# Kernel tuning notes

Measured on AMD Instinct MI355X. Metric: run time of the kernel, lower is better.

The kernel has to match this reference:

```python
import jax, jax.numpy as jnp
import numpy as np

N, DIM, H, E = 50000, 64, 8, 800000
NEG_SLOPE = 0.2


def setup_inputs() -> dict:
    key = jax.random.key(0)
    ks = jax.random.split(key, 6)
    x = jax.random.normal(ks[0], (N, DIM), dtype=jnp.float32)
    edge_index = jax.random.randint(ks[1], (2, E), 0, N, dtype=jnp.int32)
    # glorot-ish scaled params
    W = jax.random.normal(ks[2], (DIM, H * DIM), dtype=jnp.float32) * (1.0 / np.sqrt(DIM))
    att_src = jax.random.normal(ks[3], (H, DIM), dtype=jnp.float32) * (1.0 / np.sqrt(DIM))
    att_dst = jax.random.normal(ks[4], (H, DIM), dtype=jnp.float32) * (1.0 / np.sqrt(DIM))
    bias = jnp.zeros((DIM,), dtype=jnp.float32)
    return {"x": x, "edge_index": edge_index, "W": W, "att_src": att_src, "att_dst": att_dst, "bias": bias}


def reference(x, edge_index, W, att_src, att_dst, bias):
    n = x.shape[0]
    # PyG GATConv default: add self-loops
    loops = jnp.arange(n, dtype=edge_index.dtype)
    src = jnp.concatenate([edge_index[0], loops])  # [E+N]
    dst = jnp.concatenate([edge_index[1], loops])  # [E+N]
    # project: [N, H, C]
    h = (x @ W).reshape(n, H, DIM)
    # per-node attention contributions: [N, H]
    a_src = jnp.einsum("nhc,hc->nh", h, att_src)
    a_dst = jnp.einsum("nhc,hc->nh", h, att_dst)
    # per-edge logits with LeakyReLU: [E+N, H]
    logits = jax.nn.leaky_relu(a_src[src] + a_dst[dst], negative_slope=NEG_SLOPE)
    # segment softmax over incoming edges of each destination node
    seg_max = jax.ops.segment_max(logits, dst, num_segments=n)  # [N, H]
    seg_max = jnp.where(jnp.isfinite(seg_max), seg_max, 0.0)
    e = jnp.exp(logits - seg_max[dst])
    denom = jax.ops.segment_sum(e, dst, num_segments=n)  # [N, H]
    alpha = e / denom[dst]  # every node has a self-loop -> denom > 0
    # weighted messages and scatter-add: [E+N, H, C] -> [N, H, C]
    msg = h[src] * alpha[:, :, None]
    out = jax.ops.segment_sum(msg, dst, num_segments=n)
    # concat=False -> mean over heads, then bias
    return out.mean(axis=1) + bias
```

## Files before the change

### kernel.cpp

```cpp
#include <hip/hip_runtime.h>
#include <hip/hip_bf16.h>

#define NHEAD 8
#define KDIM 64
#define NCOL 512
#define NEG_SLOPE 0.2f
#define BUCKET 64
#define EPT 8

typedef short bf16x8 __attribute__((ext_vector_type(8)));
typedef float f32x4 __attribute__((ext_vector_type(4)));

__device__ inline float leaky(float x) { return fmaxf(x, NEG_SLOPE * x); }
__device__ inline float bf2f(unsigned short u) { return __uint_as_float(((unsigned)u) << 16); }
__device__ inline unsigned short f2bf(float f) {
    unsigned b = __float_as_uint(f);
    b += 0x7FFFu + ((b >> 16) & 1u);
    return (unsigned short)(b >> 16);
}

__global__ void k_wprep(const float* __restrict__ W, const float* __restrict__ att_src,
                        const float* __restrict__ att_dst,
                        float* __restrict__ WsT, float* __restrict__ WdT,
                        unsigned short* __restrict__ Bhi, unsigned short* __restrict__ Blo) {
    int tid = blockIdx.x * 256 + threadIdx.x;
    if (tid < NHEAD * KDIM) {
        int h = tid >> 6, k = tid & 63;
        float ps = 0.f, pd = 0.f;
        const float4* wp = (const float4*)(W + (size_t)k * NCOL + h * KDIM);
        const float4* sp = (const float4*)(att_src + h * KDIM);
        const float4* dp = (const float4*)(att_dst + h * KDIM);
        #pragma unroll
        for (int q = 0; q < KDIM / 4; ++q) {
            float4 wv = wp[q], sv = sp[q], dv = dp[q];
            ps += wv.x * sv.x + wv.y * sv.y + wv.z * sv.z + wv.w * sv.w;
            pd += wv.x * dv.x + wv.y * dv.y + wv.z * dv.z + wv.w * dv.w;
        }
        WsT[h * KDIM + k] = ps;
        WdT[h * KDIM + k] = pd;
    }
    if (tid < 4 * 16 * 64 * 8) {
        int j  = tid & 7;
        int l  = (tid >> 3) & 63;
        int kk = (tid >> 9) & 15;
        int ct = tid >> 13;
        int c  = ct * 16 + (l & 15);
        int hk = kk * 32 + ((l >> 4) << 3) + j;
        int h = hk >> 6, kx = hk & 63;
        float w = W[(size_t)kx * NCOL + h * KDIM + c];
        unsigned short hi = f2bf(w);
        Bhi[tid] = hi;
        Blo[tid] = f2bf(w - bf2f(hi));
    }
}

__global__ void k_xafill(const float* __restrict__ x,
                         const int* __restrict__ src, const int* __restrict__ dst,
                         const float* __restrict__ WsT, const float* __restrict__ WdT,
                         float* __restrict__ asrc, float* __restrict__ adst,
                         unsigned short* __restrict__ xb,
                         int* __restrict__ cur, unsigned short* __restrict__ bucket,
                         int n, int E, int nbx) {
    const int b = blockIdx.x;
    const int t = threadIdx.x;
    if (b < nbx) {
        int i = b * 256 + t;
        if (i >= n * NHEAD) return;
        int node = i >> 3, h = i & 7;
        const float4* xp = (const float4*)(x + (size_t)node * KDIM);
        const float4* sp = (const float4*)(WsT + h * KDIM);
        const float4* dp = (const float4*)(WdT + h * KDIM);
        float ps = 0.f, pd = 0.f;
        float4 kept0 = {0, 0, 0, 0}, kept1 = {0, 0, 0, 0};
        #pragma unroll
        for (int q = 0; q < KDIM / 4; ++q) {
            float4 xv = xp[q], sv = sp[q], dv = dp[q];
            if (q == 2 * h)     kept0 = xv;
            if (q == 2 * h + 1) kept1 = xv;
            ps += xv.x * sv.x + xv.y * sv.y + xv.z * sv.z + xv.w * sv.w;
            pd += xv.x * dv.x + xv.y * dv.y + xv.z * dv.z + xv.w * dv.w;
        }
        asrc[i] = ps;
        adst[i] = pd;
        ushort4 o0, o1;
        o0.x = f2bf(kept0.x); o0.y = f2bf(kept0.y); o0.z = f2bf(kept0.z); o0.w = f2bf(kept0.w);
        o1.x = f2bf(kept1.x); o1.y = f2bf(kept1.y); o1.z = f2bf(kept1.z); o1.w = f2bf(kept1.w);
        ushort4* op = (ushort4*)(xb + (size_t)node * KDIM + h * 8);
        op[0] = o0; op[1] = o1;
    } else {
        long long base = ((long long)(b - nbx) * 256 + t) * EPT;
        if (base + EPT <= E) {
            int4 d0 = *(const int4*)(dst + base);
            int4 d1 = *(const int4*)(dst + base + 4);
            int4 s0 = *(const int4*)(src + base);
            int4 s1 = *(const int4*)(src + base + 4);
            int dd[EPT] = {d0.x, d0.y, d0.z, d0.w, d1.x, d1.y, d1.z, d1.w};
            int ss[EPT] = {s0.x, s0.y, s0.z, s0.w, s1.x, s1.y, s1.z, s1.w};
            int pp[EPT];
            #pragma unroll
            for (int q = 0; q < EPT; ++q) pp[q] = atomicAdd(cur + dd[q], 1);
            #pragma unroll
            for (int q = 0; q < EPT; ++q)
                if (pp[q] < BUCKET)
                    bucket[(size_t)dd[q] * BUCKET + pp[q]] = (unsigned short)ss[q];
        } else {
            for (long long i = base; i < E; ++i) {
                int d = dst[i];
                int p = atomicAdd(cur + d, 1);
                if (p < BUCKET) bucket[(size_t)d * BUCKET + p] = (unsigned short)src[i];
            }
        }
    }
}

__global__ __launch_bounds__(256, 8) void k_aggproj(const unsigned short* __restrict__ bucket,
                                                    const int* __restrict__ cur,
                                                    const float* __restrict__ asrc,
                                                    const float* __restrict__ adst,
                                                    const unsigned short* __restrict__ xb,
                                                    const unsigned short* __restrict__ Bhi,
                                                    const unsigned short* __restrict__ Blo,
                                                    const float* __restrict__ bias,
                                                    float* __restrict__ out, int n) {
    __shared__ __align__(16) unsigned short Yh_l[16][520];

    const int t = threadIdx.x;
    const int w = t >> 6;
    const int lane = t & 63;
    const int base = blockIdx.x * 16;
    const int hg = lane >> 3;
    const int dly = (lane & 7) << 3;

    for (int q = 0; q < 4; ++q) {
        const int row = w * 4 + q;
        int d = base + row;
        if (d >= n) d = n - 1;

        const float myAd = adst[(size_t)d * NHEAD + hg];
        float den = 0.f;
        float y[8];
        #pragma unroll
        for (int i = 0; i < 8; ++i) y[i] = 0.f;

#define PROCU(AV, RW)                                                          \
    {                                                                          \
        float e_ = __expf(leaky((AV) + myAd));                                 \
        den += e_;                                                             \
        uint4 u_ = (RW);                                                       \
        y[0] += e_ * __uint_as_float(u_.x << 16);                              \
        y[1] += e_ * __uint_as_float(u_.x & 0xFFFF0000u);                      \
        y[2] += e_ * __uint_as_float(u_.y << 16);                              \
        y[3] += e_ * __uint_as_float(u_.y & 0xFFFF0000u);                      \
        y[4] += e_ * __uint_as_float(u_.z << 16);                              \
        y[5] += e_ * __uint_as_float(u_.z & 0xFFFF0000u);                      \
        y[6] += e_ * __uint_as_float(u_.w << 16);                              \
        y[7] += e_ * __uint_as_float(u_.w & 0xFFFF0000u);                      \
    }

        int cnt = cur[d];
        cnt = cnt < BUCKET ? cnt : BUCKET;
        int sv = (lane < cnt) ? (int)bucket[(size_t)d * BUCKET + lane] : 0;

        {
            float a = asrc[(size_t)d * NHEAD + hg];
            uint4 r = *(const uint4*)(xb + ((size_t)d << 6) + dly);
            PROCU(a, r)
        }

        int j = 0;
        for (; j + 4 <= cnt; j += 4) {
            int s0 = __shfl(sv, j);
            int s1 = __shfl(sv, j + 1);
            int s2 = __shfl(sv, j + 2);
            int s3 = __shfl(sv, j + 3);
            float a0 = asrc[(size_t)s0 * NHEAD + hg];
            float a1 = asrc[(size_t)s1 * NHEAD + hg];
            float a2 = asrc[(size_t)s2 * NHEAD + hg];
            float a3 = asrc[(size_t)s3 * NHEAD + hg];
            uint4 r0 = *(const uint4*)(xb + ((size_t)s0 << 6) + dly);
            uint4 r1 = *(const uint4*)(xb + ((size_t)s1 << 6) + dly);
            uint4 r2 = *(const uint4*)(xb + ((size_t)s2 << 6) + dly);
            uint4 r3 = *(const uint4*)(xb + ((size_t)s3 << 6) + dly);
            PROCU(a0, r0)
            PROCU(a1, r1)
            PROCU(a2, r2)
            PROCU(a3, r3)
        }
        for (; j < cnt; ++j) {
            int s = __shfl(sv, j);
            float a = asrc[(size_t)s * NHEAD + hg];
            uint4 r = *(const uint4*)(xb + ((size_t)s << 6) + dly);
            PROCU(a, r)
        }
#undef PROCU

        float inv = 1.0f / den;
        ushort4 h0, h1;
        h0.x = f2bf(y[0] * inv); h0.y = f2bf(y[1] * inv);
        h0.z = f2bf(y[2] * inv); h0.w = f2bf(y[3] * inv);
        h1.x = f2bf(y[4] * inv); h1.y = f2bf(y[5] * inv);
        h1.z = f2bf(y[6] * inv); h1.w = f2bf(y[7] * inv);
        unsigned short* yh = &Yh_l[row][hg * KDIM + dly];
        ((ushort4*)yh)[0] = h0; ((ushort4*)yh)[1] = h1;
    }

    __syncthreads();

    const bf16x8* BH = (const bf16x8*)Bhi;
    const bf16x8* BL = (const bf16x8*)Blo;
    const int ar = lane & 15;
    const int ak = (lane >> 4) << 3;

    f32x4 acc = {0.f, 0.f, 0.f, 0.f};
    #pragma unroll
    for (int kk = 0; kk < 16; ++kk) {
        bf16x8 ah = *(const bf16x8*)&Yh_l[ar][kk * 32 + ak];
        bf16x8 bh = BH[(w * 16 + kk) * 64 + lane];
        bf16x8 bl = BL[(w * 16 + kk) * 64 + lane];
        acc = __builtin_amdgcn_mfma_f32_16x16x32_bf16(ah, bh, acc, 0, 0, 0);
        acc = __builtin_amdgcn_mfma_f32_16x16x32_bf16(ah, bl, acc, 0, 0, 0);
    }

    int col = w * 16 + (lane & 15);
    float b = bias[col];
    int rbase = base + ((lane >> 4) << 2);
    #pragma unroll
    for (int r = 0; r < 4; ++r) {
        int rowg = rbase + r;
        if (rowg < n) out[(size_t)rowg * KDIM + col] = acc[r] * 0.125f + b;
    }
}

extern "C" void kernel_launch(void* const* d_in, const int* in_sizes, int n_in,
                              void* d_out, int out_size, void* d_ws, size_t ws_size,
                              hipStream_t stream) {
    const float* x       = (const float*)d_in[0];
    const int*   ei      = (const int*)d_in[1];
    const float* W       = (const float*)d_in[2];
    const float* att_src = (const float*)d_in[3];
    const float* att_dst = (const float*)d_in[4];
    const float* bias    = (const float*)d_in[5];

    const int n = in_sizes[0] / KDIM;
    const int E = in_sizes[1] / 2;
    const int* src = ei;
    const int* dst = ei + E;

    char* w = (char*)d_ws;
    unsigned short* xb  = (unsigned short*)w;  w += (size_t)n * KDIM * 2;
    unsigned short* Bhi = (unsigned short*)w;  w += (size_t)32768 * 2;
    unsigned short* Blo = (unsigned short*)w;  w += (size_t)32768 * 2;
    float* WsT  = (float*)w;                   w += (size_t)NHEAD * KDIM * 4;
    float* WdT  = (float*)w;                   w += (size_t)NHEAD * KDIM * 4;
    float* asrc = (float*)w;                   w += (size_t)n * NHEAD * 4;
    float* adst = (float*)w;                   w += (size_t)n * NHEAD * 4;
    int*   cur  = (int*)w;                     w += (size_t)n * 4;
    unsigned short* bucket = (unsigned short*)w; w += (size_t)n * BUCKET * 2;

    hipMemsetAsync(cur, 0, (size_t)n * 4, stream);

    k_wprep<<<128, 256, 0, stream>>>(W, att_src, att_dst, WsT, WdT, Bhi, Blo);

    const int nbx = (n * NHEAD + 255) / 256;
    const int ethreads = (E + EPT - 1) / EPT;
    const int nbe = (ethreads + 255) / 256;
    k_xafill<<<nbx + nbe, 256, 0, stream>>>(x, src, dst, WsT, WdT, asrc, adst, xb,
                                            cur, bucket, n, E, nbx);

    k_aggproj<<<(n + 15) / 16, 256, 0, stream>>>(bucket, cur, asrc, adst, xb, Bhi, Blo,
                                                 bias, (float*)d_out, n);
}
```

Measured before the change: 156.6 us.

## Partition bucket fill by destination-node bins to localize atomics

The edge bucketing is restructured: 256 fill blocks each take an edge slice and one of 8 destination-node bins, and a block only processes edges whose dst falls in its bin. Each edge's dst is therefore read 8 times, but the atomics and bucket writes from a block are confined to one eighth of the node range, which is meant to improve cache locality and cut atomic contention spread. The fill blocks are also placed before the projection blocks so they start first. The cost is 8x redundant reads of dst, scalar instead of vectorized loads, and a fixed block count that may underuse the GPU.

```diff
diff --git a/kernel.cpp b/kernel.cpp
--- a/kernel.cpp
+++ b/kernel.cpp
@@ -6,7 +6,7 @@
 #define NCOL 512
 #define NEG_SLOPE 0.2f
 #define BUCKET 64
-#define EPT 8
+#define NFILL 256
 
 typedef short bf16x8 __attribute__((ext_vector_type(8)));
 typedef float f32x4 __attribute__((ext_vector_type(4)));
@@ -60,13 +60,45 @@
                          float* __restrict__ asrc, float* __restrict__ adst,
                          unsigned short* __restrict__ xb,
                          int* __restrict__ cur, unsigned short* __restrict__ bucket,
-                         int n, int E, int nbx) {
+                         int n, long long E) {
     const int b = blockIdx.x;
     const int t = threadIdx.x;
-    if (b < nbx) {
-        int i = b * 256 + t;
-        if (i >= n * NHEAD) return;
-        int node = i >> 3, h = i & 7;
+
+    if (b < NFILL) {
+        const int bin   = b & 7;
+        const int slice = b >> 3;
+        const int ns = (int)(((long long)bin * n) >> 3);
+        const int ne = (int)(((long long)(bin + 1) * n) >> 3);
+        const long long e0 = (long long)slice * E / (NFILL / 8);
+        const long long e1 = (long long)(slice + 1) * E / (NFILL / 8);
+
+#define FPROC(D, I)                                                            \
+        if ((D) >= ns && (D) < ne) {                                           \
+            int p_ = atomicAdd(cur + (D), 1);                                  \
+            if (p_ < BUCKET)                                                   \
+                bucket[((size_t)(D) << 6) + p_] = (unsigned short)src[I];      \
+        }
+
+        long long i = e0 + t;
+        for (; i + 768 < e1; i += 1024) {
+            int d0 = dst[i];
+            int d1 = dst[i + 256];
+            int d2 = dst[i + 512];
+            int d3 = dst[i + 768];
+            FPROC(d0, i)
+            FPROC(d1, i + 256)
+            FPROC(d2, i + 512)
+            FPROC(d3, i + 768)
+        }
+        for (; i < e1; i += 256) {
+            int d = dst[i];
+            FPROC(d, i)
+        }
+#undef FPROC
+    } else {
+        long long i = (long long)(b - NFILL) * 256 + t;
+        if (i >= (long long)n * NHEAD) return;
+        int node = (int)(i >> 3), h = (int)(i & 7);
         const float4* xp = (const float4*)(x + (size_t)node * KDIM);
         const float4* sp = (const float4*)(WsT + h * KDIM);
         const float4* dp = (const float4*)(WdT + h * KDIM);
@@ -87,29 +119,6 @@
         o1.x = f2bf(kept1.x); o1.y = f2bf(kept1.y); o1.z = f2bf(kept1.z); o1.w = f2bf(kept1.w);
         ushort4* op = (ushort4*)(xb + (size_t)node * KDIM + h * 8);
         op[0] = o0; op[1] = o1;
-    } else {
-        long long base = ((long long)(b - nbx) * 256 + t) * EPT;
-        if (base + EPT <= E) {
-            int4 d0 = *(const int4*)(dst + base);
-            int4 d1 = *(const int4*)(dst + base + 4);
-            int4 s0 = *(const int4*)(src + base);
-            int4 s1 = *(const int4*)(src + base + 4);
-            int dd[EPT] = {d0.x, d0.y, d0.z, d0.w, d1.x, d1.y, d1.z, d1.w};
-            int ss[EPT] = {s0.x, s0.y, s0.z, s0.w, s1.x, s1.y, s1.z, s1.w};
-            int pp[EPT];
-            #pragma unroll
-            for (int q = 0; q < EPT; ++q) pp[q] = atomicAdd(cur + dd[q], 1);
-            #pragma unroll
-            for (int q = 0; q < EPT; ++q)
-                if (pp[q] < BUCKET)
-                    bucket[(size_t)dd[q] * BUCKET + pp[q]] = (unsigned short)ss[q];
-        } else {
-            for (long long i = base; i < E; ++i) {
-                int d = dst[i];
-                int p = atomicAdd(cur + d, 1);
-                if (p < BUCKET) bucket[(size_t)d * BUCKET + p] = (unsigned short)src[i];
-            }
-        }
     }
 }
 
@@ -242,7 +251,7 @@
     const float* bias    = (const float*)d_in[5];
 
     const int n = in_sizes[0] / KDIM;
-    const int E = in_sizes[1] / 2;
+    const long long E = in_sizes[1] / 2;
     const int* src = ei;
     const int* dst = ei + E;
 
@@ -261,11 +270,9 @@
 
     k_wprep<<<128, 256, 0, stream>>>(W, att_src, att_dst, WsT, WdT, Bhi, Blo);
 
-    const int nbx = (n * NHEAD + 255) / 256;
-    const int ethreads = (E + EPT - 1) / EPT;
-    const int nbe = (ethreads + 255) / 256;
-    k_xafill<<<nbx + nbe, 256, 0, stream>>>(x, src, dst, WsT, WdT, asrc, adst, xb,
-                                            cur, bucket, n, E, nbx);
+    const int nbx = (int)(((long long)n * NHEAD + 255) / 256);
+    k_xafill<<<NFILL + nbx, 256, 0, stream>>>(x, src, dst, WsT, WdT, asrc, adst, xb,
+                                              cur, bucket, n, E);
 
     k_aggproj<<<(n + 15) / 16, 256, 0, stream>>>(bucket, cur, asrc, adst, xb, Bhi, Blo,
                                                  bias, (float*)d_out, n);
```

Result: slower. 174.4 us (+11.3%).
